# Kernel tuning notes

Measured on AMD Instinct MI355X. Metric: run time of the kernel, lower is better.

The kernel has to match this reference:

```python
import jax, jax.numpy as jnp
import numpy as np

N = 100000        # nodes
E = 1600000       # edges
F_IN = 32         # raw node features
C = 128           # out_channels / hidden
L = 5             # gated graph conv layers
G = 1024          # number of graphs in batch


def setup_inputs() -> dict:
    key = jax.random.key(0)
    ks = jax.random.split(key, 12)
    x = jax.random.normal(ks[0], (N, F_IN), dtype=jnp.float32)
    edge_index = jax.random.randint(ks[1], (2, E), 0, N, dtype=jnp.int32)
    edge_weight = jax.random.uniform(ks[2], (E,), dtype=jnp.float32)
    batch = jnp.sort(jax.random.randint(ks[3], (N,), 0, G, dtype=jnp.int32))
    # parameters (scaled small, fan-in style)
    W_emb = jax.random.normal(ks[4], (F_IN, C), dtype=jnp.float32) / np.sqrt(F_IN)
    b_emb = jnp.zeros((C,), dtype=jnp.float32)
    W = jax.random.normal(ks[5], (L, C, C), dtype=jnp.float32) / np.sqrt(C)
    W_ih = jax.random.normal(ks[6], (3 * C, C), dtype=jnp.float32) / np.sqrt(C)
    W_hh = jax.random.normal(ks[7], (3 * C, C), dtype=jnp.float32) / np.sqrt(C)
    b_ih = jnp.zeros((3 * C,), dtype=jnp.float32)
    b_hh = jnp.zeros((3 * C,), dtype=jnp.float32)
    W_prop = jax.random.normal(ks[8], (C, 1), dtype=jnp.float32) / np.sqrt(C)
    b_prop = jnp.zeros((1,), dtype=jnp.float32)
    return {"x": x, "edge_index": edge_index, "edge_weight": edge_weight,
            "batch": batch, "W_emb": W_emb, "b_emb": b_emb, "W": W,
            "W_ih": W_ih, "W_hh": W_hh, "b_ih": b_ih, "b_hh": b_hh,
            "W_prop": W_prop, "b_prop": b_prop}


def _gated_graph_conv(h, src, dst, edge_weight, W, W_ih, W_hh, b_ih, b_hh):
    n_nodes = h.shape[0]

    def step(h, Wl):
        m = h @ Wl                                    # [N,C] per-layer linear
        msg = m[src] * edge_weight[:, None]           # gather + edge weight [E,C]
        agg = jax.ops.segment_sum(msg, dst, num_segments=n_nodes)  # scatter-add
        # torch GRUCell (gate order r, z, n)
        gi = agg @ W_ih.T + b_ih                      # [N,3C]
        gh = h @ W_hh.T + b_hh
        i_r, i_z, i_n = jnp.split(gi, 3, axis=-1)
        h_r, h_z, h_n = jnp.split(gh, 3, axis=-1)
        r = jax.nn.sigmoid(i_r + h_r)
        z = jax.nn.sigmoid(i_z + h_z)
        n = jnp.tanh(i_n + r * h_n)
        h_new = (1.0 - z) * n + z * h
        return h_new, None

    h, _ = jax.lax.scan(step, h, W)
    return h


def reference(x, edge_index, edge_weight, batch, W_emb, b_emb, W,
              W_ih, W_hh, b_ih, b_hh, W_prop, b_prop):
    h0 = x @ W_emb + b_emb                            # node embedding [N,C]
    src, dst = edge_index[0], edge_index[1]
    h = _gated_graph_conv(h0, src, dst, edge_weight, W, W_ih, W_hh, b_ih, b_hh)
    node_prop = h @ W_prop + b_prop                   # [N,1]
    graph_prop = jax.ops.segment_sum(node_prop, batch, num_segments=G)  # [G,1]
    return graph_prop.squeeze(1)                      # [G]
```

## Files before the change

### kernel.cpp

```cpp
#include <hip/hip_runtime.h>

#define NN 100000
#define CC 128
#define EE 1600000
#define GG 1024
#define LL 5
#define NBUCKET 12500

typedef __attribute__((ext_vector_type(8))) short bf16x8;
typedef __attribute__((ext_vector_type(4))) float f32x4;

__device__ __forceinline__ float sigmoidf_(float x) { return 1.0f / (1.0f + __expf(-x)); }
__device__ __forceinline__ float tanhf_(float x) {
  float xx = fminf(15.0f, fmaxf(-15.0f, x));
  float t = __expf(-2.0f * xx);
  return (1.0f - t) / (1.0f + t);
}
__device__ __forceinline__ unsigned short f2bf(float x) {
  unsigned int u = __float_as_uint(x);
  return (unsigned short)((u + 0x7fffu + ((u >> 16) & 1u)) >> 16);
}
__device__ __forceinline__ float bflo(unsigned int u) { return __uint_as_float(u << 16); }
__device__ __forceinline__ float bfhi(unsigned int u) { return __uint_as_float(u & 0xffff0000u); }
__device__ __forceinline__ float bf2f(unsigned short v) { return __uint_as_float((unsigned)v << 16); }


__global__ __launch_bounds__(256) void pack_kernel(
    const float* __restrict__ src, unsigned short* __restrict__ dst)
{
  int t = blockIdx.x * 256 + threadIdx.x;
  int i = t & 7, l = (t >> 3) & 63, q = t >> 9;
  int ks = q & 3, cb = q >> 2;
  int k = ks * 32 + 8 * (l >> 4) + i;
  int c = cb * 16 + (l & 15);
  dst[t] = f2bf(src[(size_t)c * CC + k]);
}

__global__ __launch_bounds__(256) void fuse_pack_kernel(
    const float* __restrict__ Wl, const float* __restrict__ W_ih,
    unsigned short* __restrict__ dst)
{
  int t = blockIdx.x * 256 + threadIdx.x;
  int i = t & 7, l = (t >> 3) & 63, q = t >> 9;
  int ks = q & 3, cb = q >> 2;
  int k = ks * 32 + 8 * (l >> 4) + i;
  int c = cb * 16 + (l & 15);
  const float* wl = Wl + (size_t)k * CC;
  const float* wi = W_ih + (size_t)c * CC;
  float acc = 0.f;
  #pragma unroll 8
  for (int j = 0; j < CC; ++j) acc = fmaf(wl[j], wi[j], acc);
  dst[t] = f2bf(acc);
}


__global__ __launch_bounds__(256) void hist_kernel(const int* __restrict__ eidx,
                                                   int* __restrict__ deg)
{
  int e = blockIdx.x * blockDim.x + threadIdx.x;
  if (e < EE) atomicAdd(&deg[eidx[EE + e]], 1);
}

__global__ __launch_bounds__(256) void scan1_kernel(const int* __restrict__ deg,
                                                    int* __restrict__ bsum)
{
  __shared__ int red[4];
  int base = blockIdx.x * 1024 + threadIdx.x * 4;
  int s = 0;
  #pragma unroll
  for (int i = 0; i < 4; ++i) { int idx = base + i; if (idx < NN) s += deg[idx]; }
  #pragma unroll
  for (int off = 32; off; off >>= 1) s += __shfl_down(s, off, 64);
  if ((threadIdx.x & 63) == 0) red[threadIdx.x >> 6] = s;
  __syncthreads();
  if (threadIdx.x == 0) bsum[blockIdx.x] = red[0] + red[1] + red[2] + red[3];
}

__global__ void scan2_kernel(int* __restrict__ bsum, int nb)
{
  if (threadIdx.x == 0 && blockIdx.x == 0) {
    int acc = 0;
    for (int i = 0; i < nb; ++i) { int v = bsum[i]; bsum[i] = acc; acc += v; }
  }
}

__global__ __launch_bounds__(256) void scan3_kernel(const int* __restrict__ deg,
                                                    const int* __restrict__ bsum,
                                                    int* __restrict__ row_ptr)
{
  __shared__ int ts[256];
  const int tid = threadIdx.x;
  const int base = blockIdx.x * 1024 + tid * 4;
  int v[4]; int s = 0;
  #pragma unroll
  for (int i = 0; i < 4; ++i) { int idx = base + i; v[i] = (idx < NN) ? deg[idx] : 0; s += v[i]; }
  ts[tid] = s; __syncthreads();
  for (int off = 1; off < 256; off <<= 1) {
    int t = (tid >= off) ? ts[tid - off] : 0;
    __syncthreads();
    ts[tid] += t;
    __syncthreads();
  }
  int excl = bsum[blockIdx.x] + ts[tid] - s;
  #pragma unroll
  for (int i = 0; i < 4; ++i) {
    int idx = base + i;
    if (idx < NN) { row_ptr[idx] = excl; excl += v[i]; }
  }
  if (blockIdx.x == 0 && tid == 0) row_ptr[NN] = EE;
}

__global__ void bcur_init_kernel(const int* __restrict__ row_ptr, int* __restrict__ bcur)
{
  int b = blockIdx.x * blockDim.x + threadIdx.x;
  if (b < NBUCKET) bcur[b] = row_ptr[b * 8];
}

__global__ __launch_bounds__(256) void fill_bucket_kernel(
    const int* __restrict__ eidx, const float* __restrict__ ew,
    int* __restrict__ bcur, int2* __restrict__ bucket)
{
  int e = blockIdx.x * blockDim.x + threadIdx.x;
  if (e < EE) {
    int d = eidx[EE + e];
    int p = atomicAdd(&bcur[d >> 3], 1);
    bucket[p] = make_int2(eidx[e] | ((d & 7) << 17), __float_as_int(ew[e]));
  }
}

__global__ __launch_bounds__(128) void fill_csr_kernel(
    const int* __restrict__ row_ptr, const int2* __restrict__ bucket,
    int2* __restrict__ csr_sw)
{
  __shared__ int cur[8];
  const int b = blockIdx.x;
  const int tid = threadIdx.x;
  if (tid < 8) cur[tid] = row_ptr[b * 8 + tid];
  __syncthreads();
  const int start = row_ptr[b * 8];
  const int stop  = row_ptr[b * 8 + 8];
  for (int j = start + tid; j < stop; j += 128) {
    int2 r = bucket[j];
    unsigned u = (unsigned)r.x;
    int p = atomicAdd(&cur[u >> 17], 1);
    csr_sw[p] = make_int2((int)(u & 0x1FFFFu), r.y);
  }
}


__global__ __launch_bounds__(128) void embed_kernel(
    const float* __restrict__ x, const float* __restrict__ W_emb,
    const float* __restrict__ b_emb, unsigned short* __restrict__ h_bf)
{
  const int node = blockIdx.x;
  const int c = threadIdx.x;
  float acc = b_emb[c];
  #pragma unroll
  for (int k = 0; k < 32; ++k)
    acc = fmaf(x[node * 32 + k], W_emb[k * CC + c], acc);
  h_bf[(size_t)node * CC + c] = f2bf(acc);
}

__global__ __launch_bounds__(256) void aggregate_kernel(
    const unsigned short* __restrict__ h_bf, const int* __restrict__ row_ptr,
    const int2* __restrict__ csr_sw, unsigned short* __restrict__ agg_bf)
{
  const int lane = threadIdx.x & 63;
  const int node = (blockIdx.x * blockDim.x + threadIdx.x) >> 6;
  if (node >= NN) return;
  const int q = lane >> 4;
  const int t = lane & 15;
  const int beg = row_ptr[node], end = row_ptr[node + 1];

  float acc[8] = {0.f, 0.f, 0.f, 0.f, 0.f, 0.f, 0.f, 0.f};
  const int last = end - 1;

  for (int j = beg; j < end; j += 16) {
    const int e0 = j + q, e1 = j + 4 + q, e2 = j + 8 + q, e3 = j + 12 + q;
    const int i0 = min(e0, last), i1 = min(e1, last);
    const int i2 = min(e2, last), i3 = min(e3, last);
    const int2 r0 = csr_sw[i0], r1 = csr_sw[i1], r2 = csr_sw[i2], r3 = csr_sw[i3];
    const float w0 = (e0 < end) ? __int_as_float(r0.y) : 0.0f;
    const float w1 = (e1 < end) ? __int_as_float(r1.y) : 0.0f;
    const float w2 = (e2 < end) ? __int_as_float(r2.y) : 0.0f;
    const float w3 = (e3 < end) ? __int_as_float(r3.y) : 0.0f;
    const uint4 u0 = *(const uint4*)(h_bf + (size_t)r0.x * CC + t * 8);
    const uint4 u1 = *(const uint4*)(h_bf + (size_t)r1.x * CC + t * 8);
    const uint4 u2 = *(const uint4*)(h_bf + (size_t)r2.x * CC + t * 8);
    const uint4 u3 = *(const uint4*)(h_bf + (size_t)r3.x * CC + t * 8);
    acc[0] = fmaf(bflo(u0.x), w0, acc[0]); acc[1] = fmaf(bfhi(u0.x), w0, acc[1]);
    acc[2] = fmaf(bflo(u0.y), w0, acc[2]); acc[3] = fmaf(bfhi(u0.y), w0, acc[3]);
    acc[4] = fmaf(bflo(u0.z), w0, acc[4]); acc[5] = fmaf(bfhi(u0.z), w0, acc[5]);
    acc[6] = fmaf(bflo(u0.w), w0, acc[6]); acc[7] = fmaf(bfhi(u0.w), w0, acc[7]);
    acc[0] = fmaf(bflo(u1.x), w1, acc[0]); acc[1] = fmaf(bfhi(u1.x), w1, acc[1]);
    acc[2] = fmaf(bflo(u1.y), w1, acc[2]); acc[3] = fmaf(bfhi(u1.y), w1, acc[3]);
    acc[4] = fmaf(bflo(u1.z), w1, acc[4]); acc[5] = fmaf(bfhi(u1.z), w1, acc[5]);
    acc[6] = fmaf(bflo(u1.w), w1, acc[6]); acc[7] = fmaf(bfhi(u1.w), w1, acc[7]);
    acc[0] = fmaf(bflo(u2.x), w2, acc[0]); acc[1] = fmaf(bfhi(u2.x), w2, acc[1]);
    acc[2] = fmaf(bflo(u2.y), w2, acc[2]); acc[3] = fmaf(bfhi(u2.y), w2, acc[3]);
    acc[4] = fmaf(bflo(u2.z), w2, acc[4]); acc[5] = fmaf(bfhi(u2.z), w2, acc[5]);
    acc[6] = fmaf(bflo(u2.w), w2, acc[6]); acc[7] = fmaf(bfhi(u2.w), w2, acc[7]);
    acc[0] = fmaf(bflo(u3.x), w3, acc[0]); acc[1] = fmaf(bfhi(u3.x), w3, acc[1]);
    acc[2] = fmaf(bflo(u3.y), w3, acc[2]); acc[3] = fmaf(bfhi(u3.y), w3, acc[3]);
    acc[4] = fmaf(bflo(u3.z), w3, acc[4]); acc[5] = fmaf(bfhi(u3.z), w3, acc[5]);
    acc[6] = fmaf(bflo(u3.w), w3, acc[6]); acc[7] = fmaf(bfhi(u3.w), w3, acc[7]);
  }

  #pragma unroll
  for (int i = 0; i < 8; ++i) {
    acc[i] += __shfl_xor(acc[i], 16, 64);
    acc[i] += __shfl_xor(acc[i], 32, 64);
  }

  if (q == 0) {
    uint4 o;
    o.x = (unsigned)f2bf(acc[0]) | ((unsigned)f2bf(acc[1]) << 16);
    o.y = (unsigned)f2bf(acc[2]) | ((unsigned)f2bf(acc[3]) << 16);
    o.z = (unsigned)f2bf(acc[4]) | ((unsigned)f2bf(acc[5]) << 16);
    o.w = (unsigned)f2bf(acc[6]) | ((unsigned)f2bf(acc[7]) << 16);
    *(uint4*)(agg_bf + (size_t)node * CC + t * 8) = o;
  }
}

__global__ __launch_bounds__(256) void gru_kernel(
    const unsigned short* __restrict__ agg_bf, unsigned short* __restrict__ h_bf,
    const unsigned short* __restrict__ Wfuse_p, const unsigned short* __restrict__ Whh_p,
    const float* __restrict__ b_ih, const float* __restrict__ b_hh)
{
  const int lane = threadIdx.x & 63;
  const int wave = threadIdx.x >> 6;
  const int node0 = blockIdx.x * 128 + wave * 32;
  if (node0 >= NN) return;
  const int col16 = lane & 15, grp = lane >> 4;

  bf16x8 aA[2][4], aH[2][4];
  #pragma unroll
  for (int t = 0; t < 2; ++t) {
    const unsigned short* arow = agg_bf + (size_t)(node0 + t * 16 + col16) * CC + grp * 8;
    const unsigned short* hrow = h_bf  + (size_t)(node0 + t * 16 + col16) * CC + grp * 8;
    #pragma unroll
    for (int ks = 0; ks < 4; ++ks) {
      aA[t][ks] = *(const bf16x8*)(arow + ks * 32);
      aH[t][ks] = *(const bf16x8*)(hrow + ks * 32);
    }
  }

  const f32x4 z4 = {0.f, 0.f, 0.f, 0.f};

  #pragma unroll
  for (int cb = 0; cb < 8; ++cb) {
    f32x4 air[2] = {z4, z4}, ahr[2] = {z4, z4};
    f32x4 aiz[2] = {z4, z4}, ahz[2] = {z4, z4};
    f32x4 ain[2] = {z4, z4}, ahn[2] = {z4, z4};
    #pragma unroll
    for (int ks = 0; ks < 4; ++ks) {
      const size_t or_ = (size_t)((cb * 4 + ks) * 64 + lane) * 8;
      const size_t oz_ = (size_t)(((8 + cb) * 4 + ks) * 64 + lane) * 8;
      const size_t on_ = (size_t)(((16 + cb) * 4 + ks) * 64 + lane) * 8;
      bf16x8 bir = *(const bf16x8*)(Wfuse_p + or_);
      bf16x8 bhr = *(const bf16x8*)(Whh_p + or_);
      bf16x8 biz = *(const bf16x8*)(Wfuse_p + oz_);
      bf16x8 bhz = *(const bf16x8*)(Whh_p + oz_);
      bf16x8 bin = *(const bf16x8*)(Wfuse_p + on_);
      bf16x8 bhn = *(const bf16x8*)(Whh_p + on_);
      #pragma unroll
      for (int t = 0; t < 2; ++t) {
        air[t] = __builtin_amdgcn_mfma_f32_16x16x32_bf16(aA[t][ks], bir, air[t], 0, 0, 0);
        ahr[t] = __builtin_amdgcn_mfma_f32_16x16x32_bf16(aH[t][ks], bhr, ahr[t], 0, 0, 0);
        aiz[t] = __builtin_amdgcn_mfma_f32_16x16x32_bf16(aA[t][ks], biz, aiz[t], 0, 0, 0);
        ahz[t] = __builtin_amdgcn_mfma_f32_16x16x32_bf16(aH[t][ks], bhz, ahz[t], 0, 0, 0);
        ain[t] = __builtin_amdgcn_mfma_f32_16x16x32_bf16(aA[t][ks], bin, ain[t], 0, 0, 0);
        ahn[t] = __builtin_amdgcn_mfma_f32_16x16x32_bf16(aH[t][ks], bhn, ahn[t], 0, 0, 0);
      }
    }
    const int o = cb * 16 + col16;
    const float bir_ = b_ih[o],       bhr_ = b_hh[o];
    const float biz_ = b_ih[128 + o], bhz_ = b_hh[128 + o];
    const float bin_ = b_ih[256 + o], bhn_ = b_hh[256 + o];
    #pragma unroll
    for (int t = 0; t < 2; ++t) {
      #pragma unroll
      for (int r = 0; r < 4; ++r) {
        float rr = sigmoidf_(air[t][r] + ahr[t][r] + bir_ + bhr_);
        float zz = sigmoidf_(aiz[t][r] + ahz[t][r] + biz_ + bhz_);
        float nn = tanhf_(ain[t][r] + bin_ + rr * (ahn[t][r] + bhn_));
        size_t idx = (size_t)(node0 + t * 16 + grp * 4 + r) * CC + o;
        float ho = bf2f(h_bf[idx]);
        h_bf[idx] = f2bf((1.0f - zz) * nn + zz * ho);
      }
    }
  }
}

__global__ __launch_bounds__(256) void prop_kernel(
    const unsigned short* __restrict__ h_bf, const int* __restrict__ batch,
    const float* __restrict__ Wp, const float* __restrict__ bp,
    float* __restrict__ out)
{
  const int lane = threadIdx.x & 63;
  const int wid = (blockIdx.x * blockDim.x + threadIdx.x) >> 6;
  const int nw = (gridDim.x * blockDim.x) >> 6;
  for (int node = wid; node < NN; node += nw) {
    unsigned int u = *(const unsigned int*)(h_bf + (size_t)node * CC + 2 * lane);
    float v = bflo(u) * Wp[2 * lane] + bfhi(u) * Wp[2 * lane + 1];
    #pragma unroll
    for (int off = 32; off > 0; off >>= 1) v += __shfl_down(v, off, 64);
    if (lane == 0) atomicAdd(&out[batch[node]], v + bp[0]);
  }
}

extern "C" void kernel_launch(void* const* d_in, const int* in_sizes, int n_in,
                              void* d_out, int out_size, void* d_ws, size_t ws_size,
                              hipStream_t stream)
{
  const float* x      = (const float*)d_in[0];
  const int*   eidx   = (const int*)d_in[1];
  const float* ew     = (const float*)d_in[2];
  const int*   batch  = (const int*)d_in[3];
  const float* W_emb  = (const float*)d_in[4];
  const float* b_emb  = (const float*)d_in[5];
  const float* W      = (const float*)d_in[6];
  const float* W_ih   = (const float*)d_in[7];
  const float* W_hh   = (const float*)d_in[8];
  const float* b_ih   = (const float*)d_in[9];
  const float* b_hh   = (const float*)d_in[10];
  const float* W_prop = (const float*)d_in[11];
  const float* b_prop = (const float*)d_in[12];
  float* out = (float*)d_out;

  char* p = (char*)d_ws;
  unsigned short* h_bf  = (unsigned short*)p; p += (size_t)NN * CC * sizeof(short);
  unsigned short* agg   = (unsigned short*)p; p += (size_t)NN * CC * sizeof(short);
  int2* csr_sw          = (int2*)p;           p += (size_t)EE * sizeof(int2);
  int2* bucket          = (int2*)p;           p += (size_t)EE * sizeof(int2);
  unsigned short* Wfuse_p = (unsigned short*)p; p += (size_t)LL * 49152 * sizeof(short);
  unsigned short* Whh_p = (unsigned short*)p; p += (size_t)49152 * sizeof(short);
  int* deg     = (int*)p;                     p += (size_t)(NN + 256) * sizeof(int);
  int* row_ptr = (int*)p;                     p += (size_t)(NN + 256) * sizeof(int);
  int* bcur    = (int*)p;                     p += (size_t)(NBUCKET + 64) * sizeof(int);
  int* bsum    = (int*)p;                     p += 1024 * sizeof(int);

  const int NB_SCAN = (NN + 1023) / 1024;
  const int EB = (EE + 255) / 256;
  const int MB2 = (NN + 127) / 128;

  pack_kernel<<<192, 256, 0, stream>>>(W_hh, Whh_p);
  for (int l = 0; l < LL; ++l)
    fuse_pack_kernel<<<192, 256, 0, stream>>>(W + (size_t)l * CC * CC, W_ih,
                                              Wfuse_p + (size_t)l * 49152);

  hipMemsetAsync(deg, 0, (size_t)NN * sizeof(int), stream);
  hist_kernel<<<EB, 256, 0, stream>>>(eidx, deg);
  scan1_kernel<<<NB_SCAN, 256, 0, stream>>>(deg, bsum);
  scan2_kernel<<<1, 64, 0, stream>>>(bsum, NB_SCAN);
  scan3_kernel<<<NB_SCAN, 256, 0, stream>>>(deg, bsum, row_ptr);
  bcur_init_kernel<<<(NBUCKET + 255) / 256, 256, 0, stream>>>(row_ptr, bcur);
  fill_bucket_kernel<<<EB, 256, 0, stream>>>(eidx, ew, bcur, bucket);
  fill_csr_kernel<<<NBUCKET, 128, 0, stream>>>(row_ptr, bucket, csr_sw);

  embed_kernel<<<NN, 128, 0, stream>>>(x, W_emb, b_emb, h_bf);

  for (int l = 0; l < LL; ++l) {
    aggregate_kernel<<<(NN + 3) / 4, 256, 0, stream>>>(h_bf, row_ptr, csr_sw, agg);
    gru_kernel<<<MB2, 256, 0, stream>>>(agg, h_bf,
                                        Wfuse_p + (size_t)l * 49152, Whh_p, b_ih, b_hh);
  }

  hipMemsetAsync(d_out, 0, (size_t)GG * sizeof(float), stream);
  prop_kernel<<<2048, 256, 0, stream>>>(h_bf, batch, W_prop, b_prop, out);
}
```

Measured before the change: 914.5 us.

## Fuse neighbor aggregation into GRU kernel via shared memory staging

Merges the aggregate and GRU kernels into one layer kernel where each wave gathers neighbor features for its 32 nodes into LDS (XOR-swizzled), then feeds them directly to the MFMA GRU. This removes the global write and re-read of the aggregated buffer and one launch per layer. Ping-pong h buffers are introduced since other blocks still read the old state. The gather now runs with one wave per 32 nodes serially, greatly reducing parallelism and latency hiding for the irregular loads.

```diff
diff --git a/kernel.cpp b/kernel.cpp
--- a/kernel.cpp
+++ b/kernel.cpp
@@ -161,86 +161,83 @@
   h_bf[(size_t)node * CC + c] = f2bf(acc);
 }
 
-__global__ __launch_bounds__(256) void aggregate_kernel(
-    const unsigned short* __restrict__ h_bf, const int* __restrict__ row_ptr,
-    const int2* __restrict__ csr_sw, unsigned short* __restrict__ agg_bf)
-{
-  const int lane = threadIdx.x & 63;
-  const int node = (blockIdx.x * blockDim.x + threadIdx.x) >> 6;
-  if (node >= NN) return;
-  const int q = lane >> 4;
-  const int t = lane & 15;
-  const int beg = row_ptr[node], end = row_ptr[node + 1];
-
-  float acc[8] = {0.f, 0.f, 0.f, 0.f, 0.f, 0.f, 0.f, 0.f};
-  const int last = end - 1;
-
-  for (int j = beg; j < end; j += 16) {
-    const int e0 = j + q, e1 = j + 4 + q, e2 = j + 8 + q, e3 = j + 12 + q;
-    const int i0 = min(e0, last), i1 = min(e1, last);
-    const int i2 = min(e2, last), i3 = min(e3, last);
-    const int2 r0 = csr_sw[i0], r1 = csr_sw[i1], r2 = csr_sw[i2], r3 = csr_sw[i3];
-    const float w0 = (e0 < end) ? __int_as_float(r0.y) : 0.0f;
-    const float w1 = (e1 < end) ? __int_as_float(r1.y) : 0.0f;
-    const float w2 = (e2 < end) ? __int_as_float(r2.y) : 0.0f;
-    const float w3 = (e3 < end) ? __int_as_float(r3.y) : 0.0f;
-    const uint4 u0 = *(const uint4*)(h_bf + (size_t)r0.x * CC + t * 8);
-    const uint4 u1 = *(const uint4*)(h_bf + (size_t)r1.x * CC + t * 8);
-    const uint4 u2 = *(const uint4*)(h_bf + (size_t)r2.x * CC + t * 8);
-    const uint4 u3 = *(const uint4*)(h_bf + (size_t)r3.x * CC + t * 8);
-    acc[0] = fmaf(bflo(u0.x), w0, acc[0]); acc[1] = fmaf(bfhi(u0.x), w0, acc[1]);
-    acc[2] = fmaf(bflo(u0.y), w0, acc[2]); acc[3] = fmaf(bfhi(u0.y), w0, acc[3]);
-    acc[4] = fmaf(bflo(u0.z), w0, acc[4]); acc[5] = fmaf(bfhi(u0.z), w0, acc[5]);
-    acc[6] = fmaf(bflo(u0.w), w0, acc[6]); acc[7] = fmaf(bfhi(u0.w), w0, acc[7]);
-    acc[0] = fmaf(bflo(u1.x), w1, acc[0]); acc[1] = fmaf(bfhi(u1.x), w1, acc[1]);
-    acc[2] = fmaf(bflo(u1.y), w1, acc[2]); acc[3] = fmaf(bfhi(u1.y), w1, acc[3]);
-    acc[4] = fmaf(bflo(u1.z), w1, acc[4]); acc[5] = fmaf(bfhi(u1.z), w1, acc[5]);
-    acc[6] = fmaf(bflo(u1.w), w1, acc[6]); acc[7] = fmaf(bfhi(u1.w), w1, acc[7]);
-    acc[0] = fmaf(bflo(u2.x), w2, acc[0]); acc[1] = fmaf(bfhi(u2.x), w2, acc[1]);
-    acc[2] = fmaf(bflo(u2.y), w2, acc[2]); acc[3] = fmaf(bfhi(u2.y), w2, acc[3]);
-    acc[4] = fmaf(bflo(u2.z), w2, acc[4]); acc[5] = fmaf(bfhi(u2.z), w2, acc[5]);
-    acc[6] = fmaf(bflo(u2.w), w2, acc[6]); acc[7] = fmaf(bfhi(u2.w), w2, acc[7]);
-    acc[0] = fmaf(bflo(u3.x), w3, acc[0]); acc[1] = fmaf(bfhi(u3.x), w3, acc[1]);
-    acc[2] = fmaf(bflo(u3.y), w3, acc[2]); acc[3] = fmaf(bfhi(u3.y), w3, acc[3]);
-    acc[4] = fmaf(bflo(u3.z), w3, acc[4]); acc[5] = fmaf(bfhi(u3.z), w3, acc[5]);
-    acc[6] = fmaf(bflo(u3.w), w3, acc[6]); acc[7] = fmaf(bfhi(u3.w), w3, acc[7]);
-  }
-
-  #pragma unroll
-  for (int i = 0; i < 8; ++i) {
-    acc[i] += __shfl_xor(acc[i], 16, 64);
-    acc[i] += __shfl_xor(acc[i], 32, 64);
-  }
-
-  if (q == 0) {
-    uint4 o;
-    o.x = (unsigned)f2bf(acc[0]) | ((unsigned)f2bf(acc[1]) << 16);
-    o.y = (unsigned)f2bf(acc[2]) | ((unsigned)f2bf(acc[3]) << 16);
-    o.z = (unsigned)f2bf(acc[4]) | ((unsigned)f2bf(acc[5]) << 16);
-    o.w = (unsigned)f2bf(acc[6]) | ((unsigned)f2bf(acc[7]) << 16);
-    *(uint4*)(agg_bf + (size_t)node * CC + t * 8) = o;
-  }
-}
-
-__global__ __launch_bounds__(256) void gru_kernel(
-    const unsigned short* __restrict__ agg_bf, unsigned short* __restrict__ h_bf,
+__global__ __launch_bounds__(256) void layer_kernel(
+    const unsigned short* __restrict__ h_in, unsigned short* __restrict__ h_out,
+    const int* __restrict__ row_ptr, const int2* __restrict__ csr_sw,
     const unsigned short* __restrict__ Wfuse_p, const unsigned short* __restrict__ Whh_p,
     const float* __restrict__ b_ih, const float* __restrict__ b_hh)
 {
+  __shared__ uint4 smem[4][32][16];
   const int lane = threadIdx.x & 63;
   const int wave = threadIdx.x >> 6;
   const int node0 = blockIdx.x * 128 + wave * 32;
   if (node0 >= NN) return;
+
+  {
+    const int q = lane >> 4;
+    const int t = lane & 15;
+    for (int nn = 0; nn < 32; ++nn) {
+      const int node = node0 + nn;
+      const int beg = row_ptr[node], end = row_ptr[node + 1];
+      const int last = end - 1;
+      float acc[8] = {0.f, 0.f, 0.f, 0.f, 0.f, 0.f, 0.f, 0.f};
+      for (int j = beg; j < end; j += 16) {
+        const int e0 = j + q, e1 = j + 4 + q, e2 = j + 8 + q, e3 = j + 12 + q;
+        const int i0 = min(e0, last), i1 = min(e1, last);
+        const int i2 = min(e2, last), i3 = min(e3, last);
+        const int2 r0 = csr_sw[i0], r1 = csr_sw[i1], r2 = csr_sw[i2], r3 = csr_sw[i3];
+        const float w0 = (e0 < end) ? __int_as_float(r0.y) : 0.0f;
+        const float w1 = (e1 < end) ? __int_as_float(r1.y) : 0.0f;
+        const float w2 = (e2 < end) ? __int_as_float(r2.y) : 0.0f;
+        const float w3 = (e3 < end) ? __int_as_float(r3.y) : 0.0f;
+        const uint4 u0 = *(const uint4*)(h_in + (size_t)r0.x * CC + t * 8);
+        const uint4 u1 = *(const uint4*)(h_in + (size_t)r1.x * CC + t * 8);
+        const uint4 u2 = *(const uint4*)(h_in + (size_t)r2.x * CC + t * 8);
+        const uint4 u3 = *(const uint4*)(h_in + (size_t)r3.x * CC + t * 8);
+        acc[0] = fmaf(bflo(u0.x), w0, acc[0]); acc[1] = fmaf(bfhi(u0.x), w0, acc[1]);
+        acc[2] = fmaf(bflo(u0.y), w0, acc[2]); acc[3] = fmaf(bfhi(u0.y), w0, acc[3]);
+        acc[4] = fmaf(bflo(u0.z), w0, acc[4]); acc[5] = fmaf(bfhi(u0.z), w0, acc[5]);
+        acc[6] = fmaf(bflo(u0.w), w0, acc[6]); acc[7] = fmaf(bfhi(u0.w), w0, acc[7]);
+        acc[0] = fmaf(bflo(u1.x), w1, acc[0]); acc[1] = fmaf(bfhi(u1.x), w1, acc[1]);
+        acc[2] = fmaf(bflo(u1.y), w1, acc[2]); acc[3] = fmaf(bfhi(u1.y), w1, acc[3]);
+        acc[4] = fmaf(bflo(u1.z), w1, acc[4]); acc[5] = fmaf(bfhi(u1.z), w1, acc[5]);
+        acc[6] = fmaf(bflo(u1.w), w1, acc[6]); acc[7] = fmaf(bfhi(u1.w), w1, acc[7]);
+        acc[0] = fmaf(bflo(u2.x), w2, acc[0]); acc[1] = fmaf(bfhi(u2.x), w2, acc[1]);
+        acc[2] = fmaf(bflo(u2.y), w2, acc[2]); acc[3] = fmaf(bfhi(u2.y), w2, acc[3]);
+        acc[4] = fmaf(bflo(u2.z), w2, acc[4]); acc[5] = fmaf(bfhi(u2.z), w2, acc[5]);
+        acc[6] = fmaf(bflo(u2.w), w2, acc[6]); acc[7] = fmaf(bfhi(u2.w), w2, acc[7]);
+        acc[0] = fmaf(bflo(u3.x), w3, acc[0]); acc[1] = fmaf(bfhi(u3.x), w3, acc[1]);
+        acc[2] = fmaf(bflo(u3.y), w3, acc[2]); acc[3] = fmaf(bfhi(u3.y), w3, acc[3]);
+        acc[4] = fmaf(bflo(u3.z), w3, acc[4]); acc[5] = fmaf(bfhi(u3.z), w3, acc[5]);
+        acc[6] = fmaf(bflo(u3.w), w3, acc[6]); acc[7] = fmaf(bfhi(u3.w), w3, acc[7]);
+      }
+      #pragma unroll
+      for (int i = 0; i < 8; ++i) {
+        acc[i] += __shfl_xor(acc[i], 16, 64);
+        acc[i] += __shfl_xor(acc[i], 32, 64);
+      }
+      if (q == 0) {
+        uint4 o;
+        o.x = (unsigned)f2bf(acc[0]) | ((unsigned)f2bf(acc[1]) << 16);
+        o.y = (unsigned)f2bf(acc[2]) | ((unsigned)f2bf(acc[3]) << 16);
+        o.z = (unsigned)f2bf(acc[4]) | ((unsigned)f2bf(acc[5]) << 16);
+        o.w = (unsigned)f2bf(acc[6]) | ((unsigned)f2bf(acc[7]) << 16);
+        smem[wave][nn][t ^ (nn & 15)] = o;
+      }
+    }
+  }
+
   const int col16 = lane & 15, grp = lane >> 4;
 
   bf16x8 aA[2][4], aH[2][4];
   #pragma unroll
   for (int t = 0; t < 2; ++t) {
-    const unsigned short* arow = agg_bf + (size_t)(node0 + t * 16 + col16) * CC + grp * 8;
-    const unsigned short* hrow = h_bf  + (size_t)(node0 + t * 16 + col16) * CC + grp * 8;
+    const int n = t * 16 + col16;
+    const unsigned short* hrow = h_in + (size_t)(node0 + n) * CC + grp * 8;
     #pragma unroll
     for (int ks = 0; ks < 4; ++ks) {
-      aA[t][ks] = *(const bf16x8*)(arow + ks * 32);
+      uint4 v = smem[wave][n][(grp + 4 * ks) ^ (n & 15)];
+      aA[t][ks] = *(bf16x8*)&v;
       aH[t][ks] = *(const bf16x8*)(hrow + ks * 32);
     }
   }
@@ -285,8 +282,8 @@
         float zz = sigmoidf_(aiz[t][r] + ahz[t][r] + biz_ + bhz_);
         float nn = tanhf_(ain[t][r] + bin_ + rr * (ahn[t][r] + bhn_));
         size_t idx = (size_t)(node0 + t * 16 + grp * 4 + r) * CC + o;
-        float ho = bf2f(h_bf[idx]);
-        h_bf[idx] = f2bf((1.0f - zz) * nn + zz * ho);
+        float ho = bf2f(h_in[idx]);
+        h_out[idx] = f2bf((1.0f - zz) * nn + zz * ho);
       }
     }
   }
@@ -329,8 +326,8 @@
   float* out = (float*)d_out;
 
   char* p = (char*)d_ws;
-  unsigned short* h_bf  = (unsigned short*)p; p += (size_t)NN * CC * sizeof(short);
-  unsigned short* agg   = (unsigned short*)p; p += (size_t)NN * CC * sizeof(short);
+  unsigned short* h0    = (unsigned short*)p; p += (size_t)NN * CC * sizeof(short);
+  unsigned short* h1    = (unsigned short*)p; p += (size_t)NN * CC * sizeof(short);
   int2* csr_sw          = (int2*)p;           p += (size_t)EE * sizeof(int2);
   int2* bucket          = (int2*)p;           p += (size_t)EE * sizeof(int2);
   unsigned short* Wfuse_p = (unsigned short*)p; p += (size_t)LL * 49152 * sizeof(short);
@@ -358,14 +355,16 @@
   fill_bucket_kernel<<<EB, 256, 0, stream>>>(eidx, ew, bcur, bucket);
   fill_csr_kernel<<<NBUCKET, 128, 0, stream>>>(row_ptr, bucket, csr_sw);
 
-  embed_kernel<<<NN, 128, 0, stream>>>(x, W_emb, b_emb, h_bf);
-
+  embed_kernel<<<NN, 128, 0, stream>>>(x, W_emb, b_emb, h0);
+
+  unsigned short* hin = h0;
+  unsigned short* hout = h1;
   for (int l = 0; l < LL; ++l) {
-    aggregate_kernel<<<(NN + 3) / 4, 256, 0, stream>>>(h_bf, row_ptr, csr_sw, agg);
-    gru_kernel<<<MB2, 256, 0, stream>>>(agg, h_bf,
-                                        Wfuse_p + (size_t)l * 49152, Whh_p, b_ih, b_hh);
+    layer_kernel<<<MB2, 256, 0, stream>>>(hin, hout, row_ptr, csr_sw,
+                                          Wfuse_p + (size_t)l * 49152, Whh_p, b_ih, b_hh);
+    unsigned short* tmp = hin; hin = hout; hout = tmp;
   }
 
   hipMemsetAsync(d_out, 0, (size_t)GG * sizeof(float), stream);
-  prop_kernel<<<2048, 256, 0, stream>>>(h_bf, batch, W_prop, b_prop, out);
-}
+  prop_kernel<<<2048, 256, 0, stream>>>(hin, batch, W_prop, b_prop, out);
+}
```

New measurement: 1.134 ms. +24.0%, slower.
